# Performance work log

Hardware: AMD Instinct MI355X
Metric: run time of the kernel (lower is better)

Reference implementation:

```python
import jax, jax.numpy as jnp
import numpy as np
from jax import lax

B, L = 128, 256
DW, DC = 100, 30
H = 400          # hidden_size (bidirectional total)
HD = H // 2      # per-direction hidden
NT = 18          # tag vocab size (BIOES)
VW, VC = 400000, 50000


def setup_inputs():
    key = jax.random.key(0)
    ks = iter(jax.random.split(key, 64))
    rn = lambda shape, s=0.1: jax.random.normal(next(ks), shape, jnp.float32) * s
    inp = {
        "words": jax.random.randint(next(ks), (B, L), 0, VW),
        "cap_words": jax.random.randint(next(ks), (B, L), 0, VC),
        "seq_len": jax.random.randint(next(ks), (B,), L // 2, L + 1),
        "target": jax.random.randint(next(ks), (B, L), 0, NT),
        "word_emb": rn((VW, DW)),
        "char_emb": rn((VC, DC)),
    }
    for l, din in ((0, DW + DC), (1, H)):
        for d in ("f", "b"):
            inp[f"W_ih_l{l}{d}"] = rn((4 * HD, din))
            inp[f"W_hh_l{l}{d}"] = rn((4 * HD, HD))
            inp[f"b_ih_l{l}{d}"] = rn((4 * HD,))
            inp[f"b_hh_l{l}{d}"] = rn((4 * HD,))
    inp["Wf"], inp["bf"] = rn((NT, HD)), jnp.zeros((NT,), jnp.float32)
    inp["Wb"], inp["bb"] = rn((NT, HD)), jnp.zeros((NT,), jnp.float32)
    inp["trans"] = rn((NT, NT))
    return inp


def _lstm_dir(x, W_ih, W_hh, b_ih, b_hh):
    # x: [B, L, D] -> hidden states [B, L, HD]; torch gate order i, f, g, o
    Bsz = x.shape[0]
    def step(carry, xt):
        h, c = carry
        g = xt @ W_ih.T + b_ih + h @ W_hh.T + b_hh
        i, f, gg, o = jnp.split(g, 4, axis=-1)
        c = jax.nn.sigmoid(f) * c + jax.nn.sigmoid(i) * jnp.tanh(gg)
        h = jax.nn.sigmoid(o) * jnp.tanh(c)
        return (h, c), h
    init = (jnp.zeros((Bsz, HD), x.dtype), jnp.zeros((Bsz, HD), x.dtype))
    _, hs = lax.scan(step, init, jnp.swapaxes(x, 0, 1))
    return jnp.swapaxes(hs, 0, 1)


def _rev(x, seq_len):
    # reverse each sequence within its true length (padding stays in place),
    # emulating pack_padded_sequence semantics for the backward direction
    t = jnp.arange(x.shape[1])[None, :]
    idx = jnp.where(t < seq_len[:, None], seq_len[:, None] - 1 - t, t)
    return jnp.take_along_axis(x, idx[:, :, None], axis=1)


def _crf_nll(logits, tags, mask, trans):
    # normalizer: forward algorithm, logsumexp scan over time with mask
    def step(alpha, inp):
        emit, m = inp  # emit: [B, NT], m: [B] bool
        new = jax.nn.logsumexp(alpha[:, :, None] + trans[None] + emit[:, None, :], axis=1)
        return jnp.where(m[:, None], new, alpha), None
    emits = jnp.swapaxes(logits, 0, 1)  # [L, B, NT]
    ms = jnp.swapaxes(mask, 0, 1)
    alpha, _ = lax.scan(step, emits[0], (emits[1:], ms[1:]))
    z = jax.nn.logsumexp(alpha, axis=1)
    # gold path score
    mf = mask.astype(logits.dtype)
    emit_sc = jnp.take_along_axis(logits, tags[:, :, None], axis=2)[:, :, 0]
    gold = jnp.sum(emit_sc * mf, axis=1) + jnp.sum(trans[tags[:, :-1], tags[:, 1:]] * mf[:, 1:], axis=1)
    return z - gold  # per-sample negative log-likelihood, shape [B]


def _model(words, cap_words, seq_len, target, word_emb, char_emb,
           W_ih_l0f, W_hh_l0f, b_ih_l0f, b_hh_l0f, W_ih_l0b, W_hh_l0b, b_ih_l0b, b_hh_l0b,
           W_ih_l1f, W_hh_l1f, b_ih_l1f, b_hh_l1f, W_ih_l1b, W_hh_l1b, b_ih_l1b, b_hh_l1b,
           Wf, bf, Wb, bb, trans):
    mask = jnp.arange(L)[None, :] < seq_len[:, None]  # [B, L] bool
    mf = mask.astype(jnp.float32)[:, :, None]
    x = jnp.concatenate([word_emb[words], char_emb[cap_words]], axis=-1)
    layers = (((W_ih_l0f, W_hh_l0f, b_ih_l0f, b_hh_l0f), (W_ih_l0b, W_hh_l0b, b_ih_l0b, b_hh_l0b)),
              ((W_ih_l1f, W_hh_l1f, b_ih_l1f, b_hh_l1f), (W_ih_l1b, W_hh_l1b, b_ih_l1b, b_hh_l1b)))
    h = x
    for fp, bp in layers:
        fwd = _lstm_dir(h, *fp)
        bwd = _rev(_lstm_dir(_rev(h, seq_len), *bp), seq_len)
        h = jnp.concatenate([fwd, bwd], axis=-1) * mf  # zero padded steps like packed LSTM
    forwards, backwards = h[..., :HD], h[..., HD:]
    logits = forwards @ Wf.T + bf + backwards @ Wb.T + bb
    return _crf_nll(logits, target, mask, trans)


def reference(words, cap_words, seq_len, target, word_emb, char_emb,
              W_ih_l0f, W_hh_l0f, b_ih_l0f, b_hh_l0f, W_ih_l0b, W_hh_l0b, b_ih_l0b, b_hh_l0b,
              W_ih_l1f, W_hh_l1f, b_ih_l1f, b_hh_l1f, W_ih_l1b, W_hh_l1b, b_ih_l1b, b_hh_l1b,
              Wf, bf, Wb, bb, trans):
    return _model(words, cap_words, seq_len, target, word_emb, char_emb,
                  W_ih_l0f, W_hh_l0f, b_ih_l0f, b_hh_l0f, W_ih_l0b, W_hh_l0b, b_ih_l0b, b_hh_l0b,
                  W_ih_l1f, W_hh_l1f, b_ih_l1f, b_hh_l1f, W_ih_l1b, W_hh_l1b, b_ih_l1b, b_hh_l1b,
                  Wf, bf, Wb, bb, trans)
```

## Files before the change

### kernel.cpp

```cpp
#include <hip/hip_runtime.h>
#include <math.h>

#define B_   128
#define L_   256
#define DW_  100
#define DC_  30
#define HD_  200
#define NT_  18
#define SG   4
#define KP0  160
#define KP1  416
#define WLP  424

typedef _Float16 half8 __attribute__((ext_vector_type(8)));
typedef _Float16 half4 __attribute__((ext_vector_type(4)));
typedef float    f32x4 __attribute__((ext_vector_type(4)));

__device__ __forceinline__ float frcp_(float x) { return __builtin_amdgcn_rcpf(x); }
__device__ __forceinline__ float sigm_(float x) { return frcp_(1.0f + __expf(-x)); }
__device__ __forceinline__ float tanh_(float x) { return 1.0f - 2.0f * frcp_(1.0f + __expf(2.0f * x)); }

__device__ __forceinline__ void barrier_lgkm() {
    asm volatile("s_waitcnt lgkmcnt(0)" ::: "memory");
    __builtin_amdgcn_s_barrier();
    asm volatile("" ::: "memory");
}

__global__ __launch_bounds__(128) void k_sortperm(const int* __restrict__ seq_len,
                                                  int* __restrict__ perm) {
    __shared__ int s[B_];
    int i = threadIdx.x;
    s[i] = seq_len[i];
    __syncthreads();
    int key = s[i], r = 0;
    for (int j = 0; j < B_; j++) {
        int v = s[j];
        r += (v < key) || (v == key && j < i);
    }
    perm[r] = i;
}

__global__ void k_embed(const int* __restrict__ words, const int* __restrict__ caps,
                        const float* __restrict__ wemb, const float* __restrict__ cemb,
                        _Float16* __restrict__ x) {
    int pos = blockIdx.x;
    int w = words[pos], c = caps[pos];
    _Float16* xp = x + (size_t)pos * KP0;
    for (int t = threadIdx.x; t < KP0; t += blockDim.x) {
        float v = 0.f;
        if (t < DW_) v = wemb[(size_t)w * DW_ + t];
        else if (t < DW_ + DC_) v = cemb[(size_t)c * DC_ + (t - DW_)];
        xp[t] = (_Float16)v;
    }
}

__global__ void k_perm_ih16(const float* __restrict__ src, _Float16* __restrict__ dst,
                            int K, int Kpad, int colOff) {
    int i = blockIdx.x * blockDim.x + threadIdx.x;
    if (i >= 800 * Kpad) return;
    int r = i / Kpad, k = i - r * Kpad;
    int jh = r % 200, g = r / 200;
    int col = colOff + (jh << 2) + g;
    dst[(size_t)col * Kpad + k] = (k < K) ? (_Float16)src[(size_t)r * K + k] : (_Float16)0.f;
}

__global__ void k_bias_perm(const float* bi_f, const float* bh_f,
                            const float* bi_b, const float* bh_b, float* bias) {
    int j = blockIdx.x * blockDim.x + threadIdx.x;
    if (j >= 1600) return;
    int dir = j / 800, r = j - dir * 800;
    int col = dir * 800 + ((r % 200) << 2) + (r / 200);
    bias[col] = dir ? (bi_b[r] + bh_b[r]) : (bi_f[r] + bh_f[r]);
}

__global__ void k_wlog(const float* __restrict__ Wf, const float* __restrict__ bfv,
                       const float* __restrict__ Wb, const float* __restrict__ bbv,
                       _Float16* __restrict__ wlB, float* __restrict__ blog) {
    int i = blockIdx.x * blockDim.x + threadIdx.x;
    if (i < 32 * WLP) {
        int n = i / WLP, k = i - n * WLP;
        float v = 0.f;
        if (n < NT_ && k < 400) v = (k < HD_) ? Wf[n * HD_ + k] : Wb[n * HD_ + (k - HD_)];
        wlB[i] = (_Float16)v;
    }
    if (i < NT_) blog[i] = bfv[i] + bbv[i];
}

__global__ __launch_bounds__(256) void k_gemm16(const _Float16* __restrict__ A,
                                                const _Float16* __restrict__ Bt,
                                                const float* __restrict__ bias,
                                                _Float16* __restrict__ C,
                                                int Kpad) {
    __shared__ __align__(16) _Float16 smem[128 * 72];
    _Float16* sA = smem;
    _Float16* sB = smem + 128 * 40;
    const int tid = threadIdx.x;
    const int w = tid >> 6, l = tid & 63, l15 = l & 15, lq = l >> 4;
    const int m0 = blockIdx.y * 128, n0 = blockIdx.x * 64;
    const int rw = (w >> 1) * 64, cw = (w & 1) * 32;
    f32x4 acc[4][2];
    #pragma unroll
    for (int i = 0; i < 4; i++)
        #pragma unroll
        for (int j = 0; j < 2; j++) acc[i][j] = f32x4{0.f, 0.f, 0.f, 0.f};

    for (int k0 = 0; k0 < Kpad; k0 += 32) {
        {
            int m = tid >> 1, c = (tid & 1) << 4;
            const _Float16* ap = A + (size_t)(m0 + m) * Kpad + k0 + c;
            *(half8*)&sA[m * 40 + c]     = *(const half8*)ap;
            *(half8*)&sA[m * 40 + c + 8] = *(const half8*)(ap + 8);
        }
        {
            int n = tid >> 2, k8 = (tid & 3) << 3;
            *(half8*)&sB[n * 40 + k8] = *(const half8*)&Bt[(size_t)(n0 + n) * Kpad + k0 + k8];
        }
        __syncthreads();
        half8 aF[4], bF[2];
        #pragma unroll
        for (int i = 0; i < 4; i++) aF[i] = *(const half8*)&sA[(rw + i * 16 + l15) * 40 + lq * 8];
        #pragma unroll
        for (int j = 0; j < 2; j++) bF[j] = *(const half8*)&sB[(cw + j * 16 + l15) * 40 + lq * 8];
        #pragma unroll
        for (int i = 0; i < 4; i++)
            #pragma unroll
            for (int j = 0; j < 2; j++)
                acc[i][j] = __builtin_amdgcn_mfma_f32_16x16x32_f16(aF[i], bF[j], acc[i][j], 0, 0, 0);
        __syncthreads();
    }

    #pragma unroll
    for (int j = 0; j < 2; j++) {
        int nl = cw + j * 16 + l15;
        float bv = bias[n0 + nl];
        #pragma unroll
        for (int i = 0; i < 4; i++) {
            int row = rw + i * 16 + lq * 4;
            #pragma unroll
            for (int r = 0; r < 4; r++)
                smem[(row + r) * 72 + nl] = (_Float16)(acc[i][j][r] + bv);
        }
    }
    __syncthreads();
    {
        int row = tid >> 1, hh = tid & 1;
        const _Float16* src = &smem[row * 72 + hh * 32];
        _Float16* dst = C + (size_t)(m0 + row) * 1600 + n0 + hh * 32;
        #pragma unroll
        for (int k = 0; k < 4; k++)
            *(half8*)(dst + k * 8) = *(const half8*)(src + k * 8);
    }
}

__global__ __launch_bounds__(1024) void k_scan14(const _Float16* __restrict__ gates,
                                                 const float* __restrict__ Whh_f,
                                                 const float* __restrict__ Whh_b,
                                                 const int* __restrict__ seq_len,
                                                 const int* __restrict__ perm,
                                                 _Float16* __restrict__ hout, int ldH) {
    const int dir = blockIdx.x & 1;
    const int b0  = (blockIdx.x >> 1) * SG;
    const int tid = threadIdx.x;
    const int w   = tid >> 6;
    const int l   = tid & 63;
    const int l15 = l & 15;
    const int lq  = l >> 4;

    __shared__ __align__(16) _Float16 hA[2][16 * 232];
    __shared__ __align__(16) _Float16 bEx[2 * 7 * 512];
    __shared__ __align__(16) float    gD[16 * 256];
    __shared__ int ssl[SG];
    __shared__ int spb[SG];

    const float* W = dir ? Whh_b : Whh_f;
    const int nT = (w < 2) ? 4 : 3;
    const int nCell = nT * 16;

    half8 Breg[3][7];
    #pragma unroll
    for (int i = 0; i < 3; i++) {
        int n  = (w * 3 + i) * 16 + l15;
        int jh = n >> 2, g = n & 3;
        const float* Wr = W + (size_t)(g * 200 + jh) * 200;
        #pragma unroll
        for (int kt = 0; kt < 7; kt++) {
            int k0 = kt * 32 + lq * 8;
            half8 f;
            #pragma unroll
            for (int j = 0; j < 8; j++) {
                int k = k0 + j;
                f[j] = (k < 200) ? (_Float16)Wr[k] : (_Float16)0.f;
            }
            Breg[i][kt] = f;
        }
    }
    if (w < 2) {
        int n  = (48 + w) * 16 + l15;
        int jh = n >> 2, g = n & 3;
        const float* Wr = W + (size_t)(g * 200 + jh) * 200;
        for (int kt = 0; kt < 7; kt++) {
            int k0 = kt * 32 + lq * 8;
            half8 f;
            for (int j = 0; j < 8; j++) {
                int k = k0 + j;
                f[j] = (k < 200) ? (_Float16)Wr[k] : (_Float16)0.f;
            }
            *(half8*)&bEx[(w * 7 + kt) * 512 + l * 8] = f;
        }
    }
    for (int i = tid; i < 2 * 16 * 232; i += 1024) (&hA[0][0])[i] = (_Float16)0.f;
    if (tid < SG) {
        int ob = perm[b0 + tid];
        spb[tid] = ob;
        ssl[tid] = seq_len[ob];
    }

    const int  v    = tid;
    const bool stv  = v < 400;
    const int  m_st = v / 100;
    const int  u_st = v - m_st * 100;

    const int cA = l;
    const bool vA = cA < nCell;
    const int iA = cA >> 4, qA = (cA >> 2) & 3, mA = cA & 3;
    const int tgA = (iA < 3) ? (w * 3 + iA) : (48 + w);
    const int hcA = tgA * 4 + qA;
    float csA = 0.f;

    __syncthreads();

    const int slmax = max(max(ssl[0], ssl[1]), max(ssl[2], ssl[3]));

    const int slA = ssl[mA];
    const int slb_st = stv ? ssl[m_st] : 0;
    const _Float16* gA_base = gates + ((size_t)spb[mA] * L_) * 1600 + dir * 800 + 4 * hcA;
    _Float16* hout_base = stv ? (hout + (size_t)spb[m_st] * L_ * ldH + dir * HD_ + 2 * u_st)
                              : hout;

    auto rowOf = [&](int t, int sl) -> int {
        return dir ? ((t < sl) ? sl - 1 - t : t) : t;
    };

    half4 gA0, gA1;
    if (vA) {
        gA0 = *(const half4*)(gA_base + (size_t)rowOf(0, slA) * 1600);
        gA1 = *(const half4*)(gA_base + (size_t)rowOf(1, slA) * 1600);
    }

    const f32x4 Cz = {0.f, 0.f, 0.f, 0.f};
    for (int t = 0; t < slmax; t++) {
        const int p = t & 1;

        if (t > 0 && stv) {
            int tp = t - 1;
            int row = dir ? ((tp < slb_st) ? slb_st - 1 - tp : tp) : tp;
            unsigned int val = (tp < slb_st) ? *(const unsigned int*)&hA[p][m_st * 232 + 2 * u_st] : 0u;
            *(unsigned int*)(hout_base + (size_t)row * ldH) = val;
        }

        f32x4 C[4];
        #pragma unroll
        for (int i = 0; i < 4; i++) C[i] = Cz;
        #pragma unroll
        for (int kt = 0; kt < 7; kt++) {
            half8 hF = *(const half8*)&hA[p][l15 * 232 + kt * 32 + lq * 8];
            #pragma unroll
            for (int i = 0; i < 3; i++)
                C[i] = __builtin_amdgcn_mfma_f32_16x16x32_f16(Breg[i][kt], hF, C[i], 0, 0, 0);
            if (w < 2) {
                half8 bF = *(const half8*)&bEx[(w * 7 + kt) * 512 + l * 8];
                C[3] = __builtin_amdgcn_mfma_f32_16x16x32_f16(bF, hF, C[3], 0, 0, 0);
            }
        }

        if (l15 < 4) {
            #pragma unroll
            for (int i = 0; i < 3; i++)
                *(f32x4*)&gD[w * 256 + (i * 16 + lq * 4 + l15) * 4] = C[i];
            if (w < 2)
                *(f32x4*)&gD[w * 256 + (3 * 16 + lq * 4 + l15) * 4] = C[3];
        }

        if (vA) {
            f32x4 gv = *(const f32x4*)&gD[w * 256 + cA * 4];
            float xi = gv[0] + (float)gA0[0];
            float xf = gv[1] + (float)gA0[1];
            float xg = gv[2] + (float)gA0[2];
            float xo = gv[3] + (float)gA0[3];
            float cn = sigm_(xf) * csA + sigm_(xi) * tanh_(xg);
            csA = cn;
            hA[1 - p][mA * 232 + hcA] = (_Float16)(sigm_(xo) * tanh_(cn));
        }

        gA0 = gA1;
        if (vA && t + 2 < L_)
            gA1 = *(const half4*)(gA_base + (size_t)rowOf(t + 2, slA) * 1600);

        barrier_lgkm();
    }
    if (stv) {
        int tp = slmax - 1;
        int row = dir ? ((tp < slb_st) ? slb_st - 1 - tp : tp) : tp;
        unsigned int val = (tp < slb_st) ? *(const unsigned int*)&hA[slmax & 1][m_st * 232 + 2 * u_st] : 0u;
        *(unsigned int*)(hout_base + (size_t)row * ldH) = val;
    }
    if (stv) {
        for (int tp = slmax; tp < L_; tp++)
            *(unsigned int*)(hout_base + (size_t)tp * ldH) = 0u;
    }
}

__global__ __launch_bounds__(256) void k_logits(const _Float16* __restrict__ h1,
                                                const _Float16* __restrict__ wlB,
                                                const float* __restrict__ blog,
                                                float* __restrict__ logits) {
    __shared__ __align__(16) _Float16 sW[32 * WLP];
    const int tid = threadIdx.x;
    const int w = tid >> 6, l = tid & 63, l15 = l & 15, lq = l >> 4;
    for (int i = tid; i < 32 * WLP / 8; i += 256)
        ((half8*)sW)[i] = ((const half8*)wlB)[i];
    __syncthreads();

    const int m0 = blockIdx.x * 64 + w * 16;
    const half8 hz = {0, 0, 0, 0, 0, 0, 0, 0};
    f32x4 acc0 = {0.f, 0.f, 0.f, 0.f}, acc1 = {0.f, 0.f, 0.f, 0.f};
    const _Float16* arow = h1 + (size_t)(m0 + l15) * 400;
    #pragma unroll
    for (int kt = 0; kt < 13; kt++) {
        int col = kt * 32 + lq * 8;
        half8 aF = (col < 400) ? *(const half8*)(arow + col) : hz;
        half8 bF0 = *(const half8*)&sW[l15 * WLP + col];
        half8 bF1 = *(const half8*)&sW[(16 + l15) * WLP + col];
        acc0 = __builtin_amdgcn_mfma_f32_16x16x32_f16(aF, bF0, acc0, 0, 0, 0);
        acc1 = __builtin_amdgcn_mfma_f32_16x16x32_f16(aF, bF1, acc1, 0, 0, 0);
    }
    {
        int n = l15;
        float bv = blog[n];
        #pragma unroll
        for (int r = 0; r < 4; r++)
            logits[(size_t)(m0 + lq * 4 + r) * NT_ + n] = acc0[r] + bv;
    }
    if (16 + l15 < NT_) {
        int n = 16 + l15;
        float bv = blog[n];
        #pragma unroll
        for (int r = 0; r < 4; r++)
            logits[(size_t)(m0 + lq * 4 + r) * NT_ + n] = acc1[r] + bv;
    }
}

__global__ __launch_bounds__(64) void k_crf(const float* __restrict__ logits,
                                            const int* __restrict__ target,
                                            const int* __restrict__ seq_len,
                                            const float* __restrict__ trans,
                                            float* __restrict__ out) {
    int b = blockIdx.x, tid = threadIdx.x;
    __shared__ float alpha[NT_];
    int sl = seq_len[b];
    const float* lg = logits + (size_t)b * L_ * NT_;
    const int* tg = target + (size_t)b * L_;

    const bool act = tid < 54;
    const int c = tid / 18, j = tid - c * 18;

    float Tl[6];
    #pragma unroll
    for (int k = 0; k < 6; k++)
        Tl[k] = act ? trans[(6 * c + k) * NT_ + j] : 0.f;

    float gacc = 0.f;
    for (int t = tid; t < L_; t += 64) {
        if (t < sl) {
            gacc += lg[t * NT_ + tg[t]];
            if (t >= 1) gacc += trans[tg[t - 1] * NT_ + tg[t]];
        }
    }
    #pragma unroll
    for (int off = 32; off; off >>= 1) gacc += __shfl_down(gacc, off);
    float gold = __shfl(gacc, 0);

    if (tid < NT_) alpha[tid] = lg[tid];

    const int src1 = (c < 2) ? tid + 18 : tid - 36;
    const int src2 = (c == 0) ? tid + 36 : tid - 18;

    for (int t = 1; t < sl; t++) {
        float m = -1e30f, s = 0.f;
        if (act) {
            float v0 = alpha[6 * c + 0] + Tl[0];
            float v1 = alpha[6 * c + 1] + Tl[1];
            float v2 = alpha[6 * c + 2] + Tl[2];
            float v3 = alpha[6 * c + 3] + Tl[3];
            float v4 = alpha[6 * c + 4] + Tl[4];
            float v5 = alpha[6 * c + 5] + Tl[5];
            m = fmaxf(fmaxf(fmaxf(v0, v1), fmaxf(v2, v3)), fmaxf(v4, v5));
            s = __expf(v0 - m) + __expf(v1 - m) + __expf(v2 - m) +
                __expf(v3 - m) + __expf(v4 - m) + __expf(v5 - m);
        }
        float m1 = __shfl(m, src1), s1 = __shfl(s, src1);
        float m2 = __shfl(m, src2), s2 = __shfl(s, src2);
        if (act && c == 0) {
            float M = fmaxf(m, fmaxf(m1, m2));
            float S = s * __expf(m - M) + s1 * __expf(m1 - M) + s2 * __expf(m2 - M);
            alpha[j] = M + __logf(S) + lg[t * NT_ + j];
        }
    }
    if (tid == 0) {
        float mx = -1e30f;
        for (int i = 0; i < NT_; i++) mx = fmaxf(mx, alpha[i]);
        float s = 0.f;
        for (int i = 0; i < NT_; i++) s += __expf(alpha[i] - mx);
        out[b] = (mx + __logf(s)) - gold;
    }
}

extern "C" void kernel_launch(void* const* d_in, const int* in_sizes, int n_in,
                              void* d_out, int out_size, void* d_ws, size_t ws_size,
                              hipStream_t stream) {
    const int*   words  = (const int*)d_in[0];
    const int*   caps   = (const int*)d_in[1];
    const int*   seq    = (const int*)d_in[2];
    const int*   target = (const int*)d_in[3];
    const float* wemb   = (const float*)d_in[4];
    const float* cemb   = (const float*)d_in[5];
    const float* Wih0f  = (const float*)d_in[6];
    const float* Whh0f  = (const float*)d_in[7];
    const float* bih0f  = (const float*)d_in[8];
    const float* bhh0f  = (const float*)d_in[9];
    const float* Wih0b  = (const float*)d_in[10];
    const float* Whh0b  = (const float*)d_in[11];
    const float* bih0b  = (const float*)d_in[12];
    const float* bhh0b  = (const float*)d_in[13];
    const float* Wih1f  = (const float*)d_in[14];
    const float* Whh1f  = (const float*)d_in[15];
    const float* bih1f  = (const float*)d_in[16];
    const float* bhh1f  = (const float*)d_in[17];
    const float* Wih1b  = (const float*)d_in[18];
    const float* Whh1b  = (const float*)d_in[19];
    const float* bih1b  = (const float*)d_in[20];
    const float* bhh1b  = (const float*)d_in[21];
    const float* Wf     = (const float*)d_in[22];
    const float* bfv    = (const float*)d_in[23];
    const float* Wb     = (const float*)d_in[24];
    const float* bbv    = (const float*)d_in[25];
    const float* trans  = (const float*)d_in[26];

    char* base = (char*)d_ws;
    _Float16* gatesH = (_Float16*)(base + 0);
    _Float16* xbuf   = (_Float16*)(base + 104857600);
    _Float16* h0b    = (_Float16*)(base + 115343360);
    _Float16* h1b    = xbuf;
    float* logitsb   = (float*)(base + 142606336);
    _Float16* wihT0  = (_Float16*)(base + 144965632);
    _Float16* wihT1  = (_Float16*)(base + 145477632);
    float* bias0     = (float*)(base + 146808832);
    float* bias1     = (float*)(base + 146815232);
    _Float16* wlB    = (_Float16*)(base + 146821632);
    float* blog      = (float*)(base + 146850432);
    int*   permb     = (int*)(base + 146850560);

    k_perm_ih16<<<(800 * KP0 + 255) / 256, 256, 0, stream>>>(Wih0f, wihT0, 130, KP0, 0);
    k_perm_ih16<<<(800 * KP0 + 255) / 256, 256, 0, stream>>>(Wih0b, wihT0, 130, KP0, 800);
    k_perm_ih16<<<(800 * KP1 + 255) / 256, 256, 0, stream>>>(Wih1f, wihT1, 400, KP1, 0);
    k_perm_ih16<<<(800 * KP1 + 255) / 256, 256, 0, stream>>>(Wih1b, wihT1, 400, KP1, 800);
    k_bias_perm<<<7, 256, 0, stream>>>(bih0f, bhh0f, bih0b, bhh0b, bias0);
    k_bias_perm<<<7, 256, 0, stream>>>(bih1f, bhh1f, bih1b, bhh1b, bias1);
    k_wlog<<<(32 * WLP + 255) / 256, 256, 0, stream>>>(Wf, bfv, Wb, bbv, wlB, blog);
    k_sortperm<<<1, 128, 0, stream>>>(seq, permb);

    k_embed<<<B_ * L_, 128, 0, stream>>>(words, caps, wemb, cemb, xbuf);

    hipMemsetAsync(h0b, 0, (size_t)32768 * KP1 * sizeof(_Float16), stream);

    k_gemm16<<<dim3(25, 256), 256, 0, stream>>>(xbuf, wihT0, bias0, gatesH, KP0);
    k_scan14<<<(B_ / SG) * 2, 1024, 0, stream>>>(gatesH, Whh0f, Whh0b, seq, permb, h0b, KP1);

    k_gemm16<<<dim3(25, 256), 256, 0, stream>>>(h0b, wihT1, bias1, gatesH, KP1);
    k_scan14<<<(B_ / SG) * 2, 1024, 0, stream>>>(gatesH, Whh1f, Whh1b, seq, permb, h1b, 400);

    k_logits<<<(B_ * L_) / 64, 256, 0, stream>>>(h1b, wlB, blog, logitsb);
    k_crf<<<B_, 64, 0, stream>>>(logitsb, target, seq, trans, (float*)d_out);
}
```

Measured before the change: 1.394 ms.

## Halve scan block size and apply LSTM gates directly from MFMA accumulators

The recurrent scan kernel drops from 16 to 8 waves per block, so each wave now holds six weight tiles in registers. The gate nonlinearities are computed straight from the MFMA accumulator lanes, which already hold the i/f/g/o values for one hidden unit and batch column. This removes the per-step LDS staging buffer and its extra read-back. The trade-off is a longer serial MFMA chain per wave, higher register pressure, and only a quarter of each wave's lanes doing the activation work.

```diff
diff --git a/kernel.cpp b/kernel.cpp
--- a/kernel.cpp
+++ b/kernel.cpp
@@ -152,12 +152,12 @@
     }
 }
 
-__global__ __launch_bounds__(1024) void k_scan14(const _Float16* __restrict__ gates,
-                                                 const float* __restrict__ Whh_f,
-                                                 const float* __restrict__ Whh_b,
-                                                 const int* __restrict__ seq_len,
-                                                 const int* __restrict__ perm,
-                                                 _Float16* __restrict__ hout, int ldH) {
+__global__ __launch_bounds__(512) void k_scan15(const _Float16* __restrict__ gates,
+                                                const float* __restrict__ Whh_f,
+                                                const float* __restrict__ Whh_b,
+                                                const int* __restrict__ seq_len,
+                                                const int* __restrict__ perm,
+                                                _Float16* __restrict__ hout, int ldH) {
     const int dir = blockIdx.x & 1;
     const int b0  = (blockIdx.x >> 1) * SG;
     const int tid = threadIdx.x;
@@ -168,18 +168,15 @@
 
     __shared__ __align__(16) _Float16 hA[2][16 * 232];
     __shared__ __align__(16) _Float16 bEx[2 * 7 * 512];
-    __shared__ __align__(16) float    gD[16 * 256];
     __shared__ int ssl[SG];
     __shared__ int spb[SG];
 
     const float* W = dir ? Whh_b : Whh_f;
-    const int nT = (w < 2) ? 4 : 3;
-    const int nCell = nT * 16;
-
-    half8 Breg[3][7];
-    #pragma unroll
-    for (int i = 0; i < 3; i++) {
-        int n  = (w * 3 + i) * 16 + l15;
+
+    half8 Breg[6][7];
+    #pragma unroll
+    for (int i = 0; i < 6; i++) {
+        int n  = (w * 6 + i) * 16 + l15;
         int jh = n >> 2, g = n & 3;
         const float* Wr = W + (size_t)(g * 200 + jh) * 200;
         #pragma unroll
@@ -208,7 +205,7 @@
             *(half8*)&bEx[(w * 7 + kt) * 512 + l * 8] = f;
         }
     }
-    for (int i = tid; i < 2 * 16 * 232; i += 1024) (&hA[0][0])[i] = (_Float16)0.f;
+    for (int i = tid; i < 2 * 16 * 232; i += 512) (&hA[0][0])[i] = (_Float16)0.f;
     if (tid < SG) {
         int ob = perm[b0 + tid];
         spb[tid] = ob;
@@ -220,20 +217,17 @@
     const int  m_st = v / 100;
     const int  u_st = v - m_st * 100;
 
-    const int cA = l;
-    const bool vA = cA < nCell;
-    const int iA = cA >> 4, qA = (cA >> 2) & 3, mA = cA & 3;
-    const int tgA = (iA < 3) ? (w * 3 + iA) : (48 + w);
-    const int hcA = tgA * 4 + qA;
-    float csA = 0.f;
+    const bool vA = l15 < 4;
+    float cs[7] = {0.f, 0.f, 0.f, 0.f, 0.f, 0.f, 0.f};
 
     __syncthreads();
 
     const int slmax = max(max(ssl[0], ssl[1]), max(ssl[2], ssl[3]));
 
-    const int slA = ssl[mA];
+    const int mb = l15 & 3;
+    const int sl_c = ssl[mb];
     const int slb_st = stv ? ssl[m_st] : 0;
-    const _Float16* gA_base = gates + ((size_t)spb[mA] * L_) * 1600 + dir * 800 + 4 * hcA;
+    const _Float16* gbase = gates + (size_t)spb[mb] * L_ * 1600 + dir * 800 + 4 * lq;
     _Float16* hout_base = stv ? (hout + (size_t)spb[m_st] * L_ * ldH + dir * HD_ + 2 * u_st)
                               : hout;
 
@@ -241,10 +235,19 @@
         return dir ? ((t < sl) ? sl - 1 - t : t) : t;
     };
 
-    half4 gA0, gA1;
+    half4 gc[7], gn[7];
     if (vA) {
-        gA0 = *(const half4*)(gA_base + (size_t)rowOf(0, slA) * 1600);
-        gA1 = *(const half4*)(gA_base + (size_t)rowOf(1, slA) * 1600);
+        const _Float16* gR0 = gbase + (size_t)rowOf(0, sl_c) * 1600;
+        const _Float16* gR1 = gbase + (size_t)rowOf(1, sl_c) * 1600;
+        #pragma unroll
+        for (int i = 0; i < 6; i++) {
+            gc[i] = *(const half4*)(gR0 + 16 * (w * 6 + i));
+            gn[i] = *(const half4*)(gR1 + 16 * (w * 6 + i));
+        }
+        if (w < 2) {
+            gc[6] = *(const half4*)(gR0 + 16 * (48 + w));
+            gn[6] = *(const half4*)(gR1 + 16 * (48 + w));
+        }
     }
 
     const f32x4 Cz = {0.f, 0.f, 0.f, 0.f};
@@ -258,43 +261,54 @@
             *(unsigned int*)(hout_base + (size_t)row * ldH) = val;
         }
 
-        f32x4 C[4];
-        #pragma unroll
-        for (int i = 0; i < 4; i++) C[i] = Cz;
+        f32x4 C[7];
+        #pragma unroll
+        for (int i = 0; i < 7; i++) C[i] = Cz;
         #pragma unroll
         for (int kt = 0; kt < 7; kt++) {
             half8 hF = *(const half8*)&hA[p][l15 * 232 + kt * 32 + lq * 8];
             #pragma unroll
-            for (int i = 0; i < 3; i++)
+            for (int i = 0; i < 6; i++)
                 C[i] = __builtin_amdgcn_mfma_f32_16x16x32_f16(Breg[i][kt], hF, C[i], 0, 0, 0);
             if (w < 2) {
                 half8 bF = *(const half8*)&bEx[(w * 7 + kt) * 512 + l * 8];
-                C[3] = __builtin_amdgcn_mfma_f32_16x16x32_f16(bF, hF, C[3], 0, 0, 0);
-            }
-        }
-
-        if (l15 < 4) {
-            #pragma unroll
-            for (int i = 0; i < 3; i++)
-                *(f32x4*)&gD[w * 256 + (i * 16 + lq * 4 + l15) * 4] = C[i];
-            if (w < 2)
-                *(f32x4*)&gD[w * 256 + (3 * 16 + lq * 4 + l15) * 4] = C[3];
+                C[6] = __builtin_amdgcn_mfma_f32_16x16x32_f16(bF, hF, C[6], 0, 0, 0);
+            }
         }
 
         if (vA) {
-            f32x4 gv = *(const f32x4*)&gD[w * 256 + cA * 4];
-            float xi = gv[0] + (float)gA0[0];
-            float xf = gv[1] + (float)gA0[1];
-            float xg = gv[2] + (float)gA0[2];
-            float xo = gv[3] + (float)gA0[3];
-            float cn = sigm_(xf) * csA + sigm_(xi) * tanh_(xg);
-            csA = cn;
-            hA[1 - p][mA * 232 + hcA] = (_Float16)(sigm_(xo) * tanh_(cn));
-        }
-
-        gA0 = gA1;
-        if (vA && t + 2 < L_)
-            gA1 = *(const half4*)(gA_base + (size_t)rowOf(t + 2, slA) * 1600);
+            #pragma unroll
+            for (int i = 0; i < 6; i++) {
+                float xi = C[i][0] + (float)gc[i][0];
+                float xf = C[i][1] + (float)gc[i][1];
+                float xg = C[i][2] + (float)gc[i][2];
+                float xo = C[i][3] + (float)gc[i][3];
+                float cn = sigm_(xf) * cs[i] + sigm_(xi) * tanh_(xg);
+                cs[i] = cn;
+                hA[1 - p][l15 * 232 + (w * 6 + i) * 4 + lq] = (_Float16)(sigm_(xo) * tanh_(cn));
+            }
+            if (w < 2) {
+                float xi = C[6][0] + (float)gc[6][0];
+                float xf = C[6][1] + (float)gc[6][1];
+                float xg = C[6][2] + (float)gc[6][2];
+                float xo = C[6][3] + (float)gc[6][3];
+                float cn = sigm_(xf) * cs[6] + sigm_(xi) * tanh_(xg);
+                cs[6] = cn;
+                hA[1 - p][l15 * 232 + (48 + w) * 4 + lq] = (_Float16)(sigm_(xo) * tanh_(cn));
+            }
+        }
+
+        if (vA) {
+            #pragma unroll
+            for (int i = 0; i < 7; i++) gc[i] = gn[i];
+            if (t + 2 < L_) {
+                const _Float16* gR2 = gbase + (size_t)rowOf(t + 2, sl_c) * 1600;
+                #pragma unroll
+                for (int i = 0; i < 6; i++)
+                    gn[i] = *(const half4*)(gR2 + 16 * (w * 6 + i));
+                if (w < 2) gn[6] = *(const half4*)(gR2 + 16 * (48 + w));
+            }
+        }
 
         barrier_lgkm();
     }
@@ -474,10 +488,10 @@
     hipMemsetAsync(h0b, 0, (size_t)32768 * KP1 * sizeof(_Float16), stream);
 
     k_gemm16<<<dim3(25, 256), 256, 0, stream>>>(xbuf, wihT0, bias0, gatesH, KP0);
-    k_scan14<<<(B_ / SG) * 2, 1024, 0, stream>>>(gatesH, Whh0f, Whh0b, seq, permb, h0b, KP1);
+    k_scan15<<<(B_ / SG) * 2, 512, 0, stream>>>(gatesH, Whh0f, Whh0b, seq, permb, h0b, KP1);
 
     k_gemm16<<<dim3(25, 256), 256, 0, stream>>>(h0b, wihT1, bias1, gatesH, KP1);
-    k_scan14<<<(B_ / SG) * 2, 1024, 0, stream>>>(gatesH, Whh1f, Whh1b, seq, permb, h1b, 400);
+    k_scan15<<<(B_ / SG) * 2, 512, 0, stream>>>(gatesH, Whh1f, Whh1b, seq, permb, h1b, 400);
 
     k_logits<<<(B_ * L_) / 64, 256, 0, stream>>>(h1b, wlB, blog, logitsb);
     k_crf<<<B_, 64, 0, stream>>>(logitsb, target, seq, trans, (float*)d_out);
```

Measured after the change: 2.465 ms. 76.9% more time.
